# Optimization experiments

Measured on AMD Instinct MI355X. Metric: run time of the kernel, lower is better.

The kernel has to match this reference:

```python
import jax, jax.numpy as jnp
import numpy as np

B, T, N, E = 4, 30, 2000, 32000
F_IN, F_HID, F_GRU, N_CLS = 8, 64, 128, 2


def setup_inputs() -> dict:
    key = jax.random.key(0)
    ks = jax.random.split(key, 12)
    return {
        "x": jax.random.normal(ks[0], (B, T, N, F_IN), jnp.float32),
        "edge_index": jax.random.randint(ks[1], (B, T, 2, E), 0, N, jnp.int32),
        "W1": jax.random.normal(ks[2], (F_IN, F_HID), jnp.float32) * 0.1,
        "b1": jax.random.normal(ks[3], (F_HID,), jnp.float32) * 0.1,
        "W2": jax.random.normal(ks[4], (F_HID, F_HID), jnp.float32) * 0.1,
        "b2": jax.random.normal(ks[5], (F_HID,), jnp.float32) * 0.1,
        "W_ih": jax.random.normal(ks[6], (3 * F_GRU, F_HID), jnp.float32) * 0.1,
        "W_hh": jax.random.normal(ks[7], (3 * F_GRU, F_GRU), jnp.float32) * 0.1,
        "b_ih": jax.random.normal(ks[8], (3 * F_GRU,), jnp.float32) * 0.1,
        "b_hh": jax.random.normal(ks[9], (3 * F_GRU,), jnp.float32) * 0.1,
        "fc_w": jax.random.normal(ks[10], (N_CLS, F_GRU), jnp.float32) * 0.1,
        "fc_b": jax.random.normal(ks[11], (N_CLS,), jnp.float32) * 0.1,
    }


def _gcn_conv(x, src, dst, W, b):
    # PyG GCNConv (edge_weight=None): add self-loops, sym-normalize, x@W, scatter-add, +bias
    n = x.shape[0]
    loops = jnp.arange(n, dtype=src.dtype)
    s = jnp.concatenate([src, loops])
    d = jnp.concatenate([dst, loops])
    deg = jax.ops.segment_sum(jnp.ones(s.shape[0], x.dtype), d, num_segments=n)
    dis = jnp.where(deg > 0, jax.lax.rsqrt(deg), 0.0)
    norm = dis[s] * dis[d]                      # [E+N]
    h = x @ W                                   # [N, Fout]
    msg = h[s] * norm[:, None]                  # gather + scale
    return jax.ops.segment_sum(msg, d, num_segments=n) + b


def _frame_embed(x, ei, W1, b1, W2, b2):
    # one graph frame -> mean-pooled 64-d embedding
    src, dst = ei[0], ei[1]
    h = jax.nn.relu(_gcn_conv(x, src, dst, W1, b1))
    h = jax.nn.relu(_gcn_conv(h, src, dst, W2, b2))
    return h.mean(axis=0)


def _gru(H, W_ih, W_hh, b_ih, b_hh):
    # H: [T, B, F_HID]; torch GRU gate order: r, z, n
    def step(h, x_t):
        gi = x_t @ W_ih.T + b_ih                # [B, 3H]
        gh = h @ W_hh.T + b_hh
        i_r, i_z, i_n = jnp.split(gi, 3, axis=-1)
        h_r, h_z, h_n = jnp.split(gh, 3, axis=-1)
        r = jax.nn.sigmoid(i_r + h_r)
        z = jax.nn.sigmoid(i_z + h_z)
        n = jnp.tanh(i_n + r * h_n)
        h_new = (1.0 - z) * n + z * h
        return h_new, None
    h0 = jnp.zeros((H.shape[1], F_GRU), H.dtype)
    h_final, _ = jax.lax.scan(step, h0, H)
    return h_final                              # [B, F_GRU]


def reference(x, edge_index, W1, b1, W2, b2, W_ih, W_hh, b_ih, b_hh, fc_w, fc_b):
    G = B * T
    xf = x.reshape(G, N, F_IN)
    eif = edge_index.reshape(G, 2, E)
    emb = jax.vmap(_frame_embed, in_axes=(0, 0, None, None, None, None))(
        xf, eif, W1, b1, W2, b2)                # [G, 64]
    H = emb.reshape(B, T, F_HID).transpose(1, 0, 2)  # [T, B, 64]
    h_final = _gru(H, W_ih, W_hh, b_ih, b_hh)   # [B, 128]
    return h_final @ fc_w.T + fc_b              # [B, 2]
```

## Files before the change

kernel.cpp:

```cpp
#include <hip/hip_runtime.h>
#include <math.h>

#define G    120
#define Nn   2000
#define Ee   32000
#define Tt   30
#define Bb   4
#define Fg   128
#define QCAP 9216
#define TSLOT 48

static __device__ __forceinline__ unsigned short f2bf(float f) {
    unsigned u = __float_as_uint(f);
    u += 0x7fffu + ((u >> 16) & 1u);
    return (unsigned short)(u >> 16);
}

#if defined(__has_builtin)
#if __has_builtin(__builtin_amdgcn_cvt_f32_fp8) && __has_builtin(__builtin_amdgcn_cvt_pk_fp8_f32)
#define HW_FP8 1
#endif
#if __has_builtin(__builtin_amdgcn_cvt_pk_f32_fp8)
#define HW_FP8_PK 1
typedef float floatx2 __attribute__((ext_vector_type(2)));
#endif
#endif

static __device__ __forceinline__ unsigned fp8_enc_sw(float x) {
    unsigned s = (__float_as_uint(x) >> 24) & 0x80u;
    float ax = fminf(fabsf(x), 448.f);
    unsigned em;
    if (ax < 0.015625f) {
        em = (unsigned)__float2int_rn(ax * 512.f);
    } else {
        int e = (int)(__float_as_uint(ax) >> 23) - 127;
        float r = ax * __uint_as_float((unsigned)((130 - e) << 23));
        int q = __float2int_rn(r);
        em = (unsigned)(((e + 7) << 3) + (q - 8));
        em = min(em, 126u);
    }
    return s | em;
}
static __device__ __forceinline__ float fp8_dec_sw(unsigned b) {
    unsigned em = b & 0x7fu;
    float mag;
    if (em < 8u) mag = (float)em * 0.001953125f;
    else mag = __uint_as_float((((em >> 3) + 120u) << 23) | ((em & 7u) << 20));
    return (b & 0x80u) ? -mag : mag;
}
static __device__ __forceinline__ unsigned fp8_pack4(float a, float b, float c, float d) {
#ifdef HW_FP8
    int w = __builtin_amdgcn_cvt_pk_fp8_f32(a, b, 0, false);
    w = __builtin_amdgcn_cvt_pk_fp8_f32(c, d, w, true);
    return (unsigned)w;
#else
    return fp8_enc_sw(a) | (fp8_enc_sw(b) << 8) | (fp8_enc_sw(c) << 16) | (fp8_enc_sw(d) << 24);
#endif
}
static __device__ __forceinline__ void fp8x4_dec(unsigned dw, float* o) {
#ifdef HW_FP8_PK
    floatx2 lo = __builtin_amdgcn_cvt_pk_f32_fp8((int)dw, false);
    floatx2 hi = __builtin_amdgcn_cvt_pk_f32_fp8((int)dw, true);
    o[0] = lo[0]; o[1] = lo[1]; o[2] = hi[0]; o[3] = hi[1];
#else
    o[0] = fp8_dec_sw(dw & 0xffu);
    o[1] = fp8_dec_sw((dw >> 8) & 0xffu);
    o[2] = fp8_dec_sw((dw >> 16) & 0xffu);
    o[3] = fp8_dec_sw((dw >> 24) & 0xffu);
#endif
}

__global__ void __launch_bounds__(1024, 1)
k_build(const int* __restrict__ ei, const float* __restrict__ x,
        float* __restrict__ dis, int* __restrict__ startA, int* __restrict__ cntA,
        int* __restrict__ csr, unsigned* __restrict__ ellT,
        float* __restrict__ aggX, float* __restrict__ emb) {
    __shared__ int   hist[Nn];
    __shared__ float disl[Nn];
    __shared__ int   ws[512];
    __shared__ int   csr_l[QCAP];
    __shared__ int   ovfS;
    int i = blockIdx.x;
    int xcd = i & 7;
    int j = i >> 3;
    int f15 = j >> 2;
    int q = j & 3;
    int g = xcd * 15 + f15;
    int gq = g * 4 + q;
    int lo = q * 500;
    int tid = threadIdx.x;
    for (int idx = tid; idx < Nn; idx += 1024) hist[idx] = 0;
    if (tid == 0) ovfS = 0;
    if (q == 0 && tid < 64) emb[g * 64 + tid] = 0.f;
    __syncthreads();
    const int* srcp = ei + (size_t)g * 2 * Ee;
    const int* dstp = srcp + Ee;
    for (int it = tid; it < Ee / 4; it += 1024) {
        int4 d = reinterpret_cast<const int4*>(dstp)[it];
        atomicAdd(&hist[d.x], 1);
        atomicAdd(&hist[d.y], 1);
        atomicAdd(&hist[d.z], 1);
        atomicAdd(&hist[d.w], 1);
    }
    __syncthreads();
    for (int idx = tid; idx < Nn; idx += 1024) disl[idx] = rsqrtf((float)hist[idx] + 1.0f);
    int cnt = 0;
    if (tid < 512) ws[tid] = (tid < 500) ? hist[lo + tid] : 0;
    if (tid < 500) cnt = hist[lo + tid];
    __syncthreads();
    for (int off = 1; off < 512; off <<= 1) {
        int v = 0;
        if (tid < 512 && tid >= off) v = ws[tid - off];
        __syncthreads();
        if (tid < 512) ws[tid] += v;
        __syncthreads();
    }
    int ex = 0;
    if (tid < 500) ex = ws[tid] - cnt;
    if (tid < 500) {
        hist[lo + tid] = ex;
        if (cnt > TSLOT - 1) atomicMax(&ovfS, 1);
    }
    __syncthreads();
    for (int it = tid; it < Ee / 4; it += 1024) {
        int4 d = reinterpret_cast<const int4*>(dstp)[it];
        int4 s = reinterpret_cast<const int4*>(srcp)[it];
        if (d.x >= lo && d.x < lo + 500) { int p = atomicAdd(&hist[d.x], 1); if (p < QCAP) csr_l[p] = s.x; }
        if (d.y >= lo && d.y < lo + 500) { int p = atomicAdd(&hist[d.y], 1); if (p < QCAP) csr_l[p] = s.y; }
        if (d.z >= lo && d.z < lo + 500) { int p = atomicAdd(&hist[d.z], 1); if (p < QCAP) csr_l[p] = s.z; }
        if (d.w >= lo && d.w < lo + 500) { int p = atomicAdd(&hist[d.w], 1); if (p < QCAP) csr_l[p] = s.w; }
    }
    __syncthreads();
    if (tid < 500) {
        int n = lo + tid;
        size_t gn = (size_t)g * Nn + n;
        cntA[gn] = cnt;
        startA[gn] = gq * QCAP + ex;
        float dn = disl[n];
        dis[gn] = dn;
        int m = min(cnt, TSLOT - 1);
        const float4* x4 = reinterpret_cast<const float4*>(x + (size_t)g * Nn * 8);
        float4 aL = {0.f, 0.f, 0.f, 0.f}, aH = {0.f, 0.f, 0.f, 0.f};
        unsigned* et = ellT + (size_t)g * TSLOT * Nn + n;
        {
            unsigned u = (unsigned)n | ((unsigned)f2bf(dn * dn) << 16);
            et[0] = u;
            float w = __uint_as_float(u & 0xffff0000u);
            float4 r0 = x4[n * 2], r1 = x4[n * 2 + 1];
            aL.x += r0.x * w; aL.y += r0.y * w; aL.z += r0.z * w; aL.w += r0.w * w;
            aH.x += r1.x * w; aH.y += r1.y * w; aH.z += r1.z * w; aH.w += r1.w * w;
        }
        for (int e = 0; e < m; ++e) {
            int s = csr_l[ex + e];
            unsigned u = (unsigned)s | ((unsigned)f2bf(disl[s] * dn) << 16);
            et[(size_t)(e + 1) * Nn] = u;
            float w = __uint_as_float(u & 0xffff0000u);
            float4 r0 = x4[s * 2], r1 = x4[s * 2 + 1];
            aL.x += r0.x * w; aL.y += r0.y * w; aL.z += r0.z * w; aL.w += r0.w * w;
            aH.x += r1.x * w; aH.y += r1.y * w; aH.z += r1.z * w; aH.w += r1.w * w;
        }
        for (int e = TSLOT - 1; e < cnt; ++e) {
            int s = csr_l[ex + e];
            float w = disl[s] * dn;
            float4 r0 = x4[s * 2], r1 = x4[s * 2 + 1];
            aL.x += r0.x * w; aL.y += r0.y * w; aL.z += r0.z * w; aL.w += r0.w * w;
            aH.x += r1.x * w; aH.y += r1.y * w; aH.z += r1.z * w; aH.w += r1.w * w;
        }
        float4* op = reinterpret_cast<float4*>(aggX + gn * 8);
        op[0] = aL; op[1] = aH;
    }
    __syncthreads();
    if (ovfS) {
        int total = ws[511];
        int* cg = csr + (size_t)gq * QCAP;
        for (int it = tid; it < total; it += 1024) cg[it] = csr_l[it];
    }
}

__global__ void __launch_bounds__(256)
k_mmf(const float* __restrict__ aggX,
      const float* __restrict__ W1, const float* __restrict__ b1,
      const float* __restrict__ W2, unsigned char* __restrict__ t2f) {
    __shared__ float Ws1[512];
    __shared__ float bs[64];
    __shared__ float xs[256];
    __shared__ float W2s[4096];
    __shared__ float h1s[32 * 65];
    int i = blockIdx.x;
    int xcd = i & 7;
    int j = i >> 3;
    int f15 = j / 63;
    int bx = j % 63;
    int g = xcd * 15 + f15;
    int tid = threadIdx.x;
    Ws1[tid]       = W1[tid];
    Ws1[tid + 256] = W1[tid + 256];
    if (tid < 64) bs[tid] = b1[tid];
#pragma unroll
    for (int k2 = 0; k2 < 16; ++k2) W2s[k2 * 256 + tid] = W2[k2 * 256 + tid];
    { int idx = bx * 256 + tid; xs[tid] = (idx < Nn * 8) ? aggX[(size_t)g * Nn * 8 + idx] : 0.f; }
    __syncthreads();
    int f = tid & 63, rr = tid >> 6;
#pragma unroll
    for (int ii = 0; ii < 8; ++ii) {
        int r = rr + 4 * ii;
        float acc = bs[f];
#pragma unroll
        for (int k = 0; k < 8; ++k) acc += xs[r * 8 + k] * Ws1[k * 64 + f];
        h1s[r * 65 + f] = fmaxf(acc, 0.f);
    }
    __syncthreads();
    int r2 = tid >> 3, fg = tid & 7;
    int n = bx * 32 + r2;
    if (n < Nn) {
        float4 a0 = {0.f, 0.f, 0.f, 0.f}, a1 = {0.f, 0.f, 0.f, 0.f};
        const float4* W24 = reinterpret_cast<const float4*>(W2s);
#pragma unroll 8
        for (int k = 0; k < 64; ++k) {
            float xv = h1s[r2 * 65 + k];
            float4 w0 = W24[k * 16 + fg * 2];
            float4 w1 = W24[k * 16 + fg * 2 + 1];
            a0.x += xv * w0.x; a0.y += xv * w0.y; a0.z += xv * w0.z; a0.w += xv * w0.w;
            a1.x += xv * w1.x; a1.y += xv * w1.y; a1.z += xv * w1.z; a1.w += xv * w1.w;
        }
        int2 ov;
        ov.x = (int)fp8_pack4(a0.x, a0.y, a0.z, a0.w);
        ov.y = (int)fp8_pack4(a1.x, a1.y, a1.z, a1.w);
        *reinterpret_cast<int2*>(t2f + ((size_t)g * Nn + n) * 64 + fg * 8) = ov;
    }
}

__global__ void __launch_bounds__(512)
k_agg64R2(const unsigned char* __restrict__ t2f, const unsigned* __restrict__ ellT,
          const int* __restrict__ cntA, const int* __restrict__ startA,
          const int* __restrict__ csr, const float* __restrict__ dis,
          const float* __restrict__ bias, float* __restrict__ emb) {
    int i = blockIdx.x;
    int xcd = i & 7;
    int j = i >> 3;
    int g = xcd * 15 + (j >> 3);
    int blk = j & 7;
    int tid = threadIdx.x;
    int w = tid >> 6;
    int lane = tid & 63;
    int ng = w >> 1;
    int half = w & 1;
    int n = blk * 256 + ng * 64 + lane;
    bool valid = (n < Nn);
    size_t gn = (size_t)g * Nn + n;
    int cnt = valid ? cntA[gn] : 0;
    int myc = valid ? (min(cnt, TSLOT - 1) + 1) : 0;
    float acc[32];
#pragma unroll
    for (int k = 0; k < 32; ++k) acc[k] = 0.f;
    const unsigned* et = ellT + (size_t)g * TSLOT * Nn + n;
    const uint4* t2g = reinterpret_cast<const uint4*>(t2f + (size_t)g * Nn * 64);
#define ROWFMA(dw, base) { float o_[4]; fp8x4_dec(dw, o_); \
    acc[base + 0] += o_[0] * wt; acc[base + 1] += o_[1] * wt; \
    acc[base + 2] += o_[2] * wt; acc[base + 3] += o_[3] * wt; }
    for (int e = 0; e < TSLOT; ++e) {
        if (!__any(e < myc)) break;
        if (e < myc) {
            unsigned p = et[(size_t)e * Nn];
            float wt = __uint_as_float(p & 0xffff0000u);
            int s = p & 0xffffu;
            const uint4* row = t2g + s * 4 + half * 2;
            uint4 r0 = row[0], r1 = row[1];
            ROWFMA(r0.x, 0)  ROWFMA(r0.y, 4)  ROWFMA(r0.z, 8)  ROWFMA(r0.w, 12)
            ROWFMA(r1.x, 16) ROWFMA(r1.y, 20) ROWFMA(r1.z, 24) ROWFMA(r1.w, 28)
        }
    }
    if (cnt > TSLOT - 1) {
        float dn = dis[gn];
        int start = startA[gn];
        const float* dsg = dis + (size_t)g * Nn;
        for (int e = TSLOT - 1; e < cnt; ++e) {
            int s = csr[start + e];
            float wt = dsg[s] * dn;
            const uint4* row = t2g + s * 4 + half * 2;
            uint4 r0 = row[0], r1 = row[1];
            ROWFMA(r0.x, 0)  ROWFMA(r0.y, 4)  ROWFMA(r0.z, 8)  ROWFMA(r0.w, 12)
            ROWFMA(r1.x, 16) ROWFMA(r1.y, 20) ROWFMA(r1.z, 24) ROWFMA(r1.w, 28)
        }
    }
#undef ROWFMA
    float mypool = 0.f;
#pragma unroll
    for (int k = 0; k < 32; ++k) {
        float v = valid ? fmaxf(acc[k] + bias[half * 32 + k], 0.f) : 0.f;
        v += __shfl_xor(v, 1);  v += __shfl_xor(v, 2);  v += __shfl_xor(v, 4);
        v += __shfl_xor(v, 8);  v += __shfl_xor(v, 16); v += __shfl_xor(v, 32);
        if (lane == k) mypool = v;
    }
    if (lane < 32) atomicAdd(&emb[g * 64 + half * 32 + lane], mypool * (1.0f / Nn));
}

__global__ void k_gi(const float* __restrict__ emb, const float* __restrict__ W_ih,
                     const float* __restrict__ b_ih, float* __restrict__ gi) {
    __shared__ float xs[64];
    int g = blockIdx.x;
    int j = threadIdx.x;
    if (j < 64) xs[j] = emb[g * 64 + j];
    __syncthreads();
    float a0 = 0.f, a1 = 0.f, a2 = 0.f, a3 = 0.f;
    const float* wr = W_ih + j * 64;
#pragma unroll
    for (int k = 0; k < 16; ++k) {
        a0 += wr[4 * k + 0] * xs[4 * k + 0];
        a1 += wr[4 * k + 1] * xs[4 * k + 1];
        a2 += wr[4 * k + 2] * xs[4 * k + 2];
        a3 += wr[4 * k + 3] * xs[4 * k + 3];
    }
    gi[(size_t)g * 384 + j] = b_ih[j] + ((a0 + a1) + (a2 + a3));
}

__global__ void __launch_bounds__(768, 1)
k_gru_seq(const float* __restrict__ gi, const float* __restrict__ W_hh,
          const float* __restrict__ b_hh, const float* __restrict__ fc_w,
          const float* __restrict__ fc_b, float* __restrict__ out) {
    __shared__ float h[Fg];
    __shared__ float part[768];
    int b = blockIdx.x;
    int tid = threadIdx.x;
    int row = tid >> 1;
    int half = tid & 1;
    float w[64];
    const float* wr = W_hh + (size_t)row * Fg + half * 64;
#pragma unroll
    for (int i = 0; i < 64; ++i) w[i] = wr[i];
    if (tid < Fg) h[tid] = 0.f;
    __syncthreads();
    for (int t = 0; t < Tt; ++t) {
        const float* hh = &h[half * 64];
        float a0 = 0.f, a1 = 0.f, a2 = 0.f, a3 = 0.f;
#pragma unroll
        for (int i = 0; i < 16; ++i) {
            a0 += w[4 * i + 0] * hh[4 * i + 0];
            a1 += w[4 * i + 1] * hh[4 * i + 1];
            a2 += w[4 * i + 2] * hh[4 * i + 2];
            a3 += w[4 * i + 3] * hh[4 * i + 3];
        }
        part[tid] = (a0 + a1) + (a2 + a3);
        __syncthreads();
        if (tid < Fg) {
            int j = tid;
            const float* gib = gi + ((size_t)b * Tt + t) * 384;
            float hr = b_hh[j]       + part[2 * j]           + part[2 * j + 1];
            float hz = b_hh[128 + j] + part[2 * (128 + j)]   + part[2 * (128 + j) + 1];
            float hn = b_hh[256 + j] + part[2 * (256 + j)]   + part[2 * (256 + j) + 1];
            float r  = 1.f / (1.f + expf(-(gib[j] + hr)));
            float z  = 1.f / (1.f + expf(-(gib[128 + j] + hz)));
            float nn = tanhf(gib[256 + j] + r * hn);
            h[j] = (1.f - z) * nn + z * h[j];
        }
        __syncthreads();
    }
    if (tid < 2) {
        float acc = fc_b[tid];
        for (int k = 0; k < Fg; ++k) acc += fc_w[tid * Fg + k] * h[k];
        out[b * 2 + tid] = acc;
    }
}

extern "C" void kernel_launch(void* const* d_in, const int* in_sizes, int n_in,
                              void* d_out, int out_size, void* d_ws, size_t ws_size,
                              hipStream_t stream) {
    const float* x     = (const float*)d_in[0];
    const int*   ei    = (const int*)  d_in[1];
    const float* W1    = (const float*)d_in[2];
    const float* b1    = (const float*)d_in[3];
    const float* W2    = (const float*)d_in[4];
    const float* b2    = (const float*)d_in[5];
    const float* W_ih  = (const float*)d_in[6];
    const float* W_hh  = (const float*)d_in[7];
    const float* b_ih  = (const float*)d_in[8];
    const float* b_hh  = (const float*)d_in[9];
    const float* fc_w  = (const float*)d_in[10];
    const float* fc_b  = (const float*)d_in[11];
    float* out = (float*)d_out;

    char* ws = (char*)d_ws;
    size_t off = 0;
    auto alloc = [&](size_t bytes) -> void* {
        void* p = ws + off;
        off = (off + bytes + 255) & ~(size_t)255;
        return p;
    };
    float*    dis    = (float*)   alloc((size_t)G * Nn * 4);
    int*      startA = (int*)     alloc((size_t)G * Nn * 4);
    int*      cntA   = (int*)     alloc((size_t)G * Nn * 4);
    int*      csr    = (int*)     alloc((size_t)G * 4 * QCAP * 4);
    unsigned* ellT   = (unsigned*)alloc((size_t)G * TSLOT * Nn * 4);
    float*    aggX   = (float*)   alloc((size_t)G * Nn * 8 * 4);
    unsigned char* t2f = (unsigned char*)alloc((size_t)G * Nn * 64);
    float*    emb    = (float*)   alloc((size_t)G * 64 * 4);
    float*    gi     = (float*)   alloc((size_t)G * 384 * 4);
    (void)ws_size; (void)in_sizes; (void)n_in; (void)out_size;

    hipLaunchKernelGGL(k_build,   dim3(480), dim3(1024), 0, stream, ei, x, dis, startA, cntA, csr, ellT, aggX, emb);
    hipLaunchKernelGGL(k_mmf,     dim3(7560), dim3(256), 0, stream, aggX, W1, b1, W2, t2f);
    hipLaunchKernelGGL(k_agg64R2, dim3(960), dim3(512), 0, stream, t2f, ellT, cntA, startA, csr, dis, b2, emb);
    hipLaunchKernelGGL(k_gi,      dim3(G), dim3(384), 0, stream, emb, W_ih, b_ih, gi);
    hipLaunchKernelGGL(k_gru_seq, dim3(Bb), dim3(768), 0, stream, gi, W_hh, b_hh, fc_w, fc_b, out);
}
```

Before: 292.2 us.

## Sort nodes by degree and fuse first-layer aggregation with both GEMMs

Build now counting-sorts each quarter's nodes by in-degree and writes the ELL table in that sorted order, along with cntS/ordS permutation arrays, so warps in the aggregation kernels handle nodes of similar degree and diverge less. The layer-1 input aggregation moves out of the build kernel into a new fused kernel, which gathers x, applies W1+ReLU and W2 in registers per node and writes fp8 rows. This removes the aggX intermediate and the separate k_mmf launch. The cost is heavy register pressure (two 64-float arrays per thread), W1/W2 read from global/cache instead of LDS, and extra shared memory and syncs in the build kernel.

New measurement: 315.6 us. +8.0%, slower.

```diff
diff --git a/kernel.cpp b/kernel.cpp
--- a/kernel.cpp
+++ b/kernel.cpp
@@ -71,14 +71,20 @@
 }
 
 __global__ void __launch_bounds__(1024, 1)
-k_build(const int* __restrict__ ei, const float* __restrict__ x,
-        float* __restrict__ dis, int* __restrict__ startA, int* __restrict__ cntA,
+k_build(const int* __restrict__ ei, float* __restrict__ dis,
+        int* __restrict__ startA, int* __restrict__ cntA,
         int* __restrict__ csr, unsigned* __restrict__ ellT,
-        float* __restrict__ aggX, float* __restrict__ emb) {
+        int* __restrict__ cntS, int* __restrict__ ordS,
+        float* __restrict__ emb) {
     __shared__ int   hist[Nn];
     __shared__ float disl[Nn];
     __shared__ int   ws[512];
     __shared__ int   csr_l[QCAP];
+    __shared__ int   cntQ[500];
+    __shared__ int   exQ[500];
+    __shared__ int   nodeAt[500];
+    __shared__ int   dh[64];
+    __shared__ int   db[64];
     __shared__ int   ovfS;
     int i = blockIdx.x;
     int xcd = i & 7;
@@ -90,6 +96,7 @@
     int lo = q * 500;
     int tid = threadIdx.x;
     for (int idx = tid; idx < Nn; idx += 1024) hist[idx] = 0;
+    if (tid < 64) dh[tid] = 0;
     if (tid == 0) ovfS = 0;
     if (q == 0 && tid < 64) emb[g * 64 + tid] = 0.f;
     __syncthreads();
@@ -119,9 +126,23 @@
     if (tid < 500) ex = ws[tid] - cnt;
     if (tid < 500) {
         hist[lo + tid] = ex;
+        cntQ[tid] = cnt;
+        exQ[tid] = ex;
         if (cnt > TSLOT - 1) atomicMax(&ovfS, 1);
-    }
-    __syncthreads();
+        atomicAdd(&dh[min(cnt, 63)], 1);
+    }
+    __syncthreads();
+    if (tid == 0) {
+        int s = 0;
+        for (int b = 0; b < 64; ++b) { db[b] = s; s += dh[b]; }
+    }
+    __syncthreads();
+    if (tid < 64) dh[tid] = db[tid];
+    __syncthreads();
+    if (tid < 500) {
+        int p = atomicAdd(&dh[min(cnt, 63)], 1);
+        nodeAt[p] = tid;
+    }
     for (int it = tid; it < Ee / 4; it += 1024) {
         int4 d = reinterpret_cast<const int4*>(dstp)[it];
         int4 s = reinterpret_cast<const int4*>(srcp)[it];
@@ -132,42 +153,27 @@
     }
     __syncthreads();
     if (tid < 500) {
-        int n = lo + tid;
-        size_t gn = (size_t)g * Nn + n;
-        cntA[gn] = cnt;
-        startA[gn] = gq * QCAP + ex;
-        float dn = disl[n];
-        dis[gn] = dn;
-        int m = min(cnt, TSLOT - 1);
-        const float4* x4 = reinterpret_cast<const float4*>(x + (size_t)g * Nn * 8);
-        float4 aL = {0.f, 0.f, 0.f, 0.f}, aH = {0.f, 0.f, 0.f, 0.f};
-        unsigned* et = ellT + (size_t)g * TSLOT * Nn + n;
-        {
-            unsigned u = (unsigned)n | ((unsigned)f2bf(dn * dn) << 16);
-            et[0] = u;
-            float w = __uint_as_float(u & 0xffff0000u);
-            float4 r0 = x4[n * 2], r1 = x4[n * 2 + 1];
-            aL.x += r0.x * w; aL.y += r0.y * w; aL.z += r0.z * w; aL.w += r0.w * w;
-            aH.x += r1.x * w; aH.y += r1.y * w; aH.z += r1.z * w; aH.w += r1.w * w;
-        }
-        for (int e = 0; e < m; ++e) {
-            int s = csr_l[ex + e];
-            unsigned u = (unsigned)s | ((unsigned)f2bf(disl[s] * dn) << 16);
-            et[(size_t)(e + 1) * Nn] = u;
-            float w = __uint_as_float(u & 0xffff0000u);
-            float4 r0 = x4[s * 2], r1 = x4[s * 2 + 1];
-            aL.x += r0.x * w; aL.y += r0.y * w; aL.z += r0.z * w; aL.w += r0.w * w;
-            aH.x += r1.x * w; aH.y += r1.y * w; aH.z += r1.z * w; aH.w += r1.w * w;
-        }
-        for (int e = TSLOT - 1; e < cnt; ++e) {
-            int s = csr_l[ex + e];
-            float w = disl[s] * dn;
-            float4 r0 = x4[s * 2], r1 = x4[s * 2 + 1];
-            aL.x += r0.x * w; aL.y += r0.y * w; aL.z += r0.z * w; aL.w += r0.w * w;
-            aH.x += r1.x * w; aH.y += r1.y * w; aH.z += r1.z * w; aH.w += r1.w * w;
-        }
-        float4* op = reinterpret_cast<float4*>(aggX + gn * 8);
-        op[0] = aL; op[1] = aH;
+        int n_own = lo + tid;
+        size_t gn_own = (size_t)g * Nn + n_own;
+        cntA[gn_own] = cnt;
+        startA[gn_own] = gq * QCAP + ex;
+        dis[gn_own] = disl[n_own];
+        int sl = nodeAt[tid];
+        int n2 = lo + sl;
+        int cnt2 = cntQ[sl];
+        int ex2 = exQ[sl];
+        int c = q * 500 + tid;
+        size_t gc = (size_t)g * Nn + c;
+        cntS[gc] = cnt2;
+        ordS[gc] = n2;
+        float dn2 = disl[n2];
+        unsigned* et = ellT + (size_t)g * TSLOT * Nn + c;
+        et[0] = (unsigned)n2 | ((unsigned)f2bf(dn2 * dn2) << 16);
+        int m2 = min(cnt2, TSLOT - 1);
+        for (int e = 0; e < m2; ++e) {
+            int s = csr_l[ex2 + e];
+            et[(size_t)(e + 1) * Nn] = (unsigned)s | ((unsigned)f2bf(disl[s] * dn2) << 16);
+        }
     }
     __syncthreads();
     if (ovfS) {
@@ -178,63 +184,122 @@
 }
 
 __global__ void __launch_bounds__(256)
-k_mmf(const float* __restrict__ aggX,
-      const float* __restrict__ W1, const float* __restrict__ b1,
-      const float* __restrict__ W2, unsigned char* __restrict__ t2f) {
-    __shared__ float Ws1[512];
-    __shared__ float bs[64];
-    __shared__ float xs[256];
-    __shared__ float W2s[4096];
-    __shared__ float h1s[32 * 65];
+k_fused(const float* __restrict__ x, const unsigned* __restrict__ ellT,
+        const int* __restrict__ cntS, const int* __restrict__ ordS,
+        const int* __restrict__ startA, const int* __restrict__ csr,
+        const float* __restrict__ dis,
+        const float* __restrict__ W1, const float* __restrict__ b1,
+        const float* __restrict__ W2, unsigned char* __restrict__ t2f) {
     int i = blockIdx.x;
     int xcd = i & 7;
     int j = i >> 3;
-    int f15 = j / 63;
-    int bx = j % 63;
-    int g = xcd * 15 + f15;
-    int tid = threadIdx.x;
-    Ws1[tid]       = W1[tid];
-    Ws1[tid + 256] = W1[tid + 256];
-    if (tid < 64) bs[tid] = b1[tid];
-#pragma unroll
-    for (int k2 = 0; k2 < 16; ++k2) W2s[k2 * 256 + tid] = W2[k2 * 256 + tid];
-    { int idx = bx * 256 + tid; xs[tid] = (idx < Nn * 8) ? aggX[(size_t)g * Nn * 8 + idx] : 0.f; }
-    __syncthreads();
-    int f = tid & 63, rr = tid >> 6;
-#pragma unroll
-    for (int ii = 0; ii < 8; ++ii) {
-        int r = rr + 4 * ii;
-        float acc = bs[f];
-#pragma unroll
-        for (int k = 0; k < 8; ++k) acc += xs[r * 8 + k] * Ws1[k * 64 + f];
-        h1s[r * 65 + f] = fmaxf(acc, 0.f);
-    }
-    __syncthreads();
-    int r2 = tid >> 3, fg = tid & 7;
-    int n = bx * 32 + r2;
-    if (n < Nn) {
-        float4 a0 = {0.f, 0.f, 0.f, 0.f}, a1 = {0.f, 0.f, 0.f, 0.f};
-        const float4* W24 = reinterpret_cast<const float4*>(W2s);
-#pragma unroll 8
+    int g = xcd * 15 + (j >> 3);
+    int blk = j & 7;
+    int p = blk * 256 + threadIdx.x;
+    bool valid = (p < Nn);
+    size_t gp = (size_t)g * Nn + (valid ? p : 0);
+    int n = valid ? ordS[gp] : 0;
+    int cnt = valid ? cntS[gp] : 0;
+    int myc = valid ? (min(cnt, TSLOT - 1) + 1) : 0;
+    float aX[8];
+#pragma unroll
+    for (int k = 0; k < 8; ++k) aX[k] = 0.f;
+    {
+        const unsigned* et = ellT + (size_t)g * TSLOT * Nn + (valid ? p : 0);
+        const float4* x4 = reinterpret_cast<const float4*>(x + (size_t)g * Nn * 8);
+        for (int e = 0; e < TSLOT; ++e) {
+            if (!__any(e < myc)) break;
+            if (e < myc) {
+                unsigned u = et[(size_t)e * Nn];
+                float w = __uint_as_float(u & 0xffff0000u);
+                int s = u & 0xffffu;
+                float4 r0 = x4[s * 2], r1 = x4[s * 2 + 1];
+                aX[0] += r0.x * w; aX[1] += r0.y * w; aX[2] += r0.z * w; aX[3] += r0.w * w;
+                aX[4] += r1.x * w; aX[5] += r1.y * w; aX[6] += r1.z * w; aX[7] += r1.w * w;
+            }
+        }
+        if (cnt > TSLOT - 1) {
+            size_t gn = (size_t)g * Nn + n;
+            float dn = dis[gn];
+            int start = startA[gn];
+            const float* dsg = dis + (size_t)g * Nn;
+            for (int e = TSLOT - 1; e < cnt; ++e) {
+                int s = csr[start + e];
+                float w = dsg[s] * dn;
+                float4 r0 = x4[s * 2], r1 = x4[s * 2 + 1];
+                aX[0] += r0.x * w; aX[1] += r0.y * w; aX[2] += r0.z * w; aX[3] += r0.w * w;
+                aX[4] += r1.x * w; aX[5] += r1.y * w; aX[6] += r1.z * w; aX[7] += r1.w * w;
+            }
+        }
+    }
+    float h1r[64];
+    {
+        const float4* b14 = reinterpret_cast<const float4*>(b1);
+#pragma unroll
+        for (int f4 = 0; f4 < 16; ++f4) {
+            float4 b = b14[f4];
+            h1r[4 * f4 + 0] = b.x; h1r[4 * f4 + 1] = b.y;
+            h1r[4 * f4 + 2] = b.z; h1r[4 * f4 + 3] = b.w;
+        }
+        const float4* W14 = reinterpret_cast<const float4*>(W1);
+#pragma unroll
+        for (int k = 0; k < 8; ++k) {
+            float hk = aX[k];
+#pragma unroll
+            for (int f4 = 0; f4 < 16; ++f4) {
+                float4 w = W14[k * 16 + f4];
+                h1r[4 * f4 + 0] += hk * w.x; h1r[4 * f4 + 1] += hk * w.y;
+                h1r[4 * f4 + 2] += hk * w.z; h1r[4 * f4 + 3] += hk * w.w;
+            }
+        }
+#pragma unroll
+        for (int f = 0; f < 64; ++f) h1r[f] = fmaxf(h1r[f], 0.f);
+    }
+    float acc2[64];
+#pragma unroll
+    for (int f = 0; f < 64; ++f) acc2[f] = 0.f;
+    {
+        const float4* W24 = reinterpret_cast<const float4*>(W2);
+#pragma unroll 4
         for (int k = 0; k < 64; ++k) {
-            float xv = h1s[r2 * 65 + k];
-            float4 w0 = W24[k * 16 + fg * 2];
-            float4 w1 = W24[k * 16 + fg * 2 + 1];
-            a0.x += xv * w0.x; a0.y += xv * w0.y; a0.z += xv * w0.z; a0.w += xv * w0.w;
-            a1.x += xv * w1.x; a1.y += xv * w1.y; a1.z += xv * w1.z; a1.w += xv * w1.w;
-        }
-        int2 ov;
-        ov.x = (int)fp8_pack4(a0.x, a0.y, a0.z, a0.w);
-        ov.y = (int)fp8_pack4(a1.x, a1.y, a1.z, a1.w);
-        *reinterpret_cast<int2*>(t2f + ((size_t)g * Nn + n) * 64 + fg * 8) = ov;
+            float hk = h1r[k];
+#pragma unroll
+            for (int f4 = 0; f4 < 16; ++f4) {
+                float4 w = W24[k * 16 + f4];
+                acc2[4 * f4 + 0] += hk * w.x; acc2[4 * f4 + 1] += hk * w.y;
+                acc2[4 * f4 + 2] += hk * w.z; acc2[4 * f4 + 3] += hk * w.w;
+            }
+        }
+    }
+    if (valid) {
+        uint4 o0, o1, o2, o3;
+        o0.x = fp8_pack4(acc2[0],  acc2[1],  acc2[2],  acc2[3]);
+        o0.y = fp8_pack4(acc2[4],  acc2[5],  acc2[6],  acc2[7]);
+        o0.z = fp8_pack4(acc2[8],  acc2[9],  acc2[10], acc2[11]);
+        o0.w = fp8_pack4(acc2[12], acc2[13], acc2[14], acc2[15]);
+        o1.x = fp8_pack4(acc2[16], acc2[17], acc2[18], acc2[19]);
+        o1.y = fp8_pack4(acc2[20], acc2[21], acc2[22], acc2[23]);
+        o1.z = fp8_pack4(acc2[24], acc2[25], acc2[26], acc2[27]);
+        o1.w = fp8_pack4(acc2[28], acc2[29], acc2[30], acc2[31]);
+        o2.x = fp8_pack4(acc2[32], acc2[33], acc2[34], acc2[35]);
+        o2.y = fp8_pack4(acc2[36], acc2[37], acc2[38], acc2[39]);
+        o2.z = fp8_pack4(acc2[40], acc2[41], acc2[42], acc2[43]);
+        o2.w = fp8_pack4(acc2[44], acc2[45], acc2[46], acc2[47]);
+        o3.x = fp8_pack4(acc2[48], acc2[49], acc2[50], acc2[51]);
+        o3.y = fp8_pack4(acc2[52], acc2[53], acc2[54], acc2[55]);
+        o3.z = fp8_pack4(acc2[56], acc2[57], acc2[58], acc2[59]);
+        o3.w = fp8_pack4(acc2[60], acc2[61], acc2[62], acc2[63]);
+        uint4* op = reinterpret_cast<uint4*>(t2f + ((size_t)g * Nn + n) * 64);
+        op[0] = o0; op[1] = o1; op[2] = o2; op[3] = o3;
     }
 }
 
 __global__ void __launch_bounds__(512)
-k_agg64R2(const unsigned char* __restrict__ t2f, const unsigned* __restrict__ ellT,
-          const int* __restrict__ cntA, const int* __restrict__ startA,
-          const int* __restrict__ csr, const float* __restrict__ dis,
-          const float* __restrict__ bias, float* __restrict__ emb) {
+k_agg64R3(const unsigned char* __restrict__ t2f, const unsigned* __restrict__ ellT,
+          const int* __restrict__ cntS, const int* __restrict__ ordS,
+          const int* __restrict__ startA, const int* __restrict__ csr,
+          const float* __restrict__ dis, const float* __restrict__ bias,
+          float* __restrict__ emb) {
     int i = blockIdx.x;
     int xcd = i & 7;
     int j = i >> 3;
@@ -245,15 +310,15 @@
     int lane = tid & 63;
     int ng = w >> 1;
     int half = w & 1;
-    int n = blk * 256 + ng * 64 + lane;
-    bool valid = (n < Nn);
-    size_t gn = (size_t)g * Nn + n;
-    int cnt = valid ? cntA[gn] : 0;
+    int p = blk * 256 + ng * 64 + lane;
+    bool valid = (p < Nn);
+    size_t gp = (size_t)g * Nn + (valid ? p : 0);
+    int cnt = valid ? cntS[gp] : 0;
     int myc = valid ? (min(cnt, TSLOT - 1) + 1) : 0;
     float acc[32];
 #pragma unroll
     for (int k = 0; k < 32; ++k) acc[k] = 0.f;
-    const unsigned* et = ellT + (size_t)g * TSLOT * Nn + n;
+    const unsigned* et = ellT + (size_t)g * TSLOT * Nn + (valid ? p : 0);
     const uint4* t2g = reinterpret_cast<const uint4*>(t2f + (size_t)g * Nn * 64);
 #define ROWFMA(dw, base) { float o_[4]; fp8x4_dec(dw, o_); \
     acc[base + 0] += o_[0] * wt; acc[base + 1] += o_[1] * wt; \
@@ -261,9 +326,9 @@
     for (int e = 0; e < TSLOT; ++e) {
         if (!__any(e < myc)) break;
         if (e < myc) {
-            unsigned p = et[(size_t)e * Nn];
-            float wt = __uint_as_float(p & 0xffff0000u);
-            int s = p & 0xffffu;
+            unsigned u = et[(size_t)e * Nn];
+            float wt = __uint_as_float(u & 0xffff0000u);
+            int s = u & 0xffffu;
             const uint4* row = t2g + s * 4 + half * 2;
             uint4 r0 = row[0], r1 = row[1];
             ROWFMA(r0.x, 0)  ROWFMA(r0.y, 4)  ROWFMA(r0.z, 8)  ROWFMA(r0.w, 12)
@@ -271,6 +336,8 @@
         }
     }
     if (cnt > TSLOT - 1) {
+        int n = ordS[gp];
+        size_t gn = (size_t)g * Nn + n;
         float dn = dis[gn];
         int start = startA[gn];
         const float* dsg = dis + (size_t)g * Nn;
@@ -389,17 +456,18 @@
     float*    dis    = (float*)   alloc((size_t)G * Nn * 4);
     int*      startA = (int*)     alloc((size_t)G * Nn * 4);
     int*      cntA   = (int*)     alloc((size_t)G * Nn * 4);
+    int*      cntS   = (int*)     alloc((size_t)G * Nn * 4);
+    int*      ordS   = (int*)     alloc((size_t)G * Nn * 4);
     int*      csr    = (int*)     alloc((size_t)G * 4 * QCAP * 4);
     unsigned* ellT   = (unsigned*)alloc((size_t)G * TSLOT * Nn * 4);
-    float*    aggX   = (float*)   alloc((size_t)G * Nn * 8 * 4);
     unsigned char* t2f = (unsigned char*)alloc((size_t)G * Nn * 64);
     float*    emb    = (float*)   alloc((size_t)G * 64 * 4);
     float*    gi     = (float*)   alloc((size_t)G * 384 * 4);
     (void)ws_size; (void)in_sizes; (void)n_in; (void)out_size;
 
-    hipLaunchKernelGGL(k_build,   dim3(480), dim3(1024), 0, stream, ei, x, dis, startA, cntA, csr, ellT, aggX, emb);
-    hipLaunchKernelGGL(k_mmf,     dim3(7560), dim3(256), 0, stream, aggX, W1, b1, W2, t2f);
-    hipLaunchKernelGGL(k_agg64R2, dim3(960), dim3(512), 0, stream, t2f, ellT, cntA, startA, csr, dis, b2, emb);
+    hipLaunchKernelGGL(k_build,   dim3(480), dim3(1024), 0, stream, ei, dis, startA, cntA, csr, ellT, cntS, ordS, emb);
+    hipLaunchKernelGGL(k_fused,   dim3(960), dim3(256), 0, stream, x, ellT, cntS, ordS, startA, csr, dis, W1, b1, W2, t2f);
+    hipLaunchKernelGGL(k_agg64R3, dim3(960), dim3(512), 0, stream, t2f, ellT, cntS, ordS, startA, csr, dis, b2, emb);
     hipLaunchKernelGGL(k_gi,      dim3(G), dim3(384), 0, stream, emb, W_ih, b_ih, gi);
     hipLaunchKernelGGL(k_gru_seq, dim3(Bb), dim3(768), 0, stream, gi, W_hh, b_hh, fc_w, fc_b, out);
 }
```
